# Optimization experiments

Hardware: AMD Instinct MI355X
Metric: run time of the kernel (lower is better)

The kernel has to match this reference:

```python
import jax, jax.numpy as jnp
import numpy as np

B, C, H, W = 64, 64, 64, 64
KD = 64  # kernel_dim == res == dim (required by the torch reshapes)


def _ln(t, g, b, eps=1e-5):
    mu = jnp.mean(t, axis=-1, keepdims=True)
    var = jnp.var(t, axis=-1, keepdims=True)
    return (t - mu) * jax.lax.rsqrt(var + eps) * g + b


def _cos_map(n, kd):
    i = jnp.arange(n, dtype=jnp.float32)[:, None]
    j = jnp.arange(kd, dtype=jnp.float32)[None, :]
    return jnp.cos(i * j * jnp.pi / n) / kd


def setup_inputs() -> dict:
    key = jax.random.key(0)
    ks = jax.random.split(key, 6)
    s = 0.02
    return {
        "x": jax.random.normal(ks[0], (B, C, H, W), jnp.float32),
        "freq_embed": jax.random.normal(ks[1], (H, W, C), jnp.float32),
        "g_k": jnp.ones((C,), jnp.float32), "b_k": jnp.zeros((C,), jnp.float32),
        "Wk": jax.random.normal(ks[2], (C, KD), jnp.float32) * s, "bk": jnp.zeros((KD,), jnp.float32),
        "g_z": jnp.ones((C,), jnp.float32), "b_z": jnp.zeros((C,), jnp.float32),
        "Wz": jax.random.normal(ks[3], (C, C), jnp.float32) * s, "bz": jnp.zeros((C,), jnp.float32),
        "g_o": jnp.ones((KD,), jnp.float32), "b_o": jnp.zeros((KD,), jnp.float32),
        "Wo": jax.random.normal(ks[4], (KD, C), jnp.float32) * s, "bo": jnp.zeros((C,), jnp.float32),
    }


def reference(x, freq_embed, g_k, b_k, Wk, bk, g_z, b_z, Wz, bz, g_o, b_o, Wo, bo):
    # x: (B,C,H,W) -> (B,H,W,C), matching the torch permute branch
    x = jnp.transpose(x, (0, 2, 3, 1))
    Bc, Hc, Wc, Cc = x.shape
    kd = Wk.shape[1]
    xin = x + freq_embed[None]                    # freq_embed broadcast over batch
    k = _ln(xin, g_k, b_k) @ Wk + bk              # (B,H,W,kd)
    z = _ln(freq_embed, g_z, b_z) @ Wz + bz       # to_k(freq_embed): (H,W,C)
    cosn = _cos_map(Hc, kd)                       # (H,kd)
    cosm = _cos_map(Wc, kd)                       # (W,kd)
    i = jnp.arange(Hc, dtype=jnp.float32)[:, None]
    j = jnp.arange(Wc, dtype=jnp.float32)[None, :]
    decay = (jnp.exp(-(i + j) / max(Hc, Wc)) / kd).astype(x.dtype)  # (H,W)
    wexp = decay[:, :, None] ** z                 # (H,W,C), decay > 0
    # separable forward DCT (two kernel-1 conv1d == two contractions)
    t = jnp.einsum('nh,bhwc->bnwc', cosn, k)
    t = jnp.einsum('mw,bnwc->bnmc', cosm, t)
    t = t * wexp[None]                            # exponential-decay spectral gate
    # separable inverse DCT
    t = jnp.einsum('nh,bnmc->bhmc', cosn, t)
    t = jnp.einsum('mw,bhmc->bhwc', cosm, t)
    out = _ln(t, g_o, b_o) * jax.nn.silu(z)[None]
    out = out @ Wo + bo
    return jnp.transpose(out, (0, 3, 1, 2))       # back to BCHW
```

## Files before the change

kernel.cpp:

```cpp
#include <hip/hip_runtime.h>


#define PL_ST 4160
#define TC_ST 4160

typedef __attribute__((ext_vector_type(8))) short short8;
typedef __attribute__((ext_vector_type(4))) float f32x4;
typedef __attribute__((ext_vector_type(4))) unsigned short us4;

__device__ __forceinline__ unsigned short bfhi(float f) {
    return (unsigned short)(__builtin_bit_cast(unsigned int, f) >> 16);
}
__device__ __forceinline__ float hif(float f) {
    return __builtin_bit_cast(float, __builtin_bit_cast(unsigned int, f) & 0xFFFF0000u);
}
__device__ __forceinline__ int swa(int row, int col) {
    return (row << 7) + (((col >> 3) ^ (row & 7)) << 4) + ((col & 7) << 1);
}
__device__ __forceinline__ short8 fragrd(const short* buf, int row, int kc) {
    int a = (row << 7) + ((kc ^ (row & 7)) << 4);
    return *(const short8*)((const char*)buf + a);
}
__device__ __forceinline__ f32x4 mm3(short8 ah, short8 al, short8 bh, short8 bl, f32x4 acc) {
    acc = __builtin_amdgcn_mfma_f32_16x16x32_bf16(ah, bh, acc, 0, 0, 0);
    acc = __builtin_amdgcn_mfma_f32_16x16x32_bf16(ah, bl, acc, 0, 0, 0);
    acc = __builtin_amdgcn_mfma_f32_16x16x32_bf16(al, bh, acc, 0, 0, 0);
    return acc;
}

__device__ __forceinline__ void mm_block(const short* Ah, const short* Al,
                                         const short* Bh, const short* Bl,
                                         int m0, int n0, int l15, int q,
                                         f32x4 (&acc)[2][2]) {
    const f32x4 zero = {0.f, 0.f, 0.f, 0.f};
    acc[0][0] = zero; acc[0][1] = zero; acc[1][0] = zero; acc[1][1] = zero;
    #pragma unroll
    for (int kb = 0; kb < 2; ++kb) {
        int kc = (kb << 2) + q;
        short8 a0h = fragrd(Ah, m0 + l15, kc);
        short8 a0l = fragrd(Al, m0 + l15, kc);
        short8 a1h = fragrd(Ah, m0 + 16 + l15, kc);
        short8 a1l = fragrd(Al, m0 + 16 + l15, kc);
        short8 b0h = fragrd(Bh, n0 + l15, kc);
        short8 b0l = fragrd(Bl, n0 + l15, kc);
        short8 b1h = fragrd(Bh, n0 + 16 + l15, kc);
        short8 b1l = fragrd(Bl, n0 + 16 + l15, kc);
        acc[0][0] = mm3(a0h, a0l, b0h, b0l, acc[0][0]);
        acc[0][1] = mm3(a0h, a0l, b1h, b1l, acc[0][1]);
        acc[1][0] = mm3(a1h, a1l, b0h, b0l, acc[1][0]);
        acc[1][1] = mm3(a1h, a1l, b1h, b1l, acc[1][1]);
    }
}

__device__ __forceinline__ void mm_block_regB(const short* Ah, const short* Al,
                                              const short8 (&bf)[2][2][2],
                                              int m0, int l15, int q,
                                              f32x4 (&acc)[2][2]) {
    const f32x4 zero = {0.f, 0.f, 0.f, 0.f};
    acc[0][0] = zero; acc[0][1] = zero; acc[1][0] = zero; acc[1][1] = zero;
    #pragma unroll
    for (int kb = 0; kb < 2; ++kb) {
        int kc = (kb << 2) + q;
        short8 a0h = fragrd(Ah, m0 + l15, kc);
        short8 a0l = fragrd(Al, m0 + l15, kc);
        short8 a1h = fragrd(Ah, m0 + 16 + l15, kc);
        short8 a1l = fragrd(Al, m0 + 16 + l15, kc);
        #pragma unroll
        for (int u = 0; u < 2; ++u) {
            acc[0][u] = mm3(a0h, a0l, bf[u][kb][0], bf[u][kb][1], acc[0][u]);
            acc[1][u] = mm3(a1h, a1l, bf[u][kb][0], bf[u][kb][1], acc[1][u]);
        }
    }
}

__global__ __launch_bounds__(256) void k_pre1(
    const float* __restrict__ g_k, const float* __restrict__ b_k,
    const float* __restrict__ Wk, const float* __restrict__ bk,
    const float* __restrict__ g_z, const float* __restrict__ b_z,
    const float* __restrict__ Wz, const float* __restrict__ bz,
    const float* __restrict__ Wo,
    unsigned short* __restrict__ WkTh, unsigned short* __restrict__ WkTl,
    float* __restrict__ su_k, float* __restrict__ v_k,
    unsigned short* __restrict__ WzTh, unsigned short* __restrict__ WzTl,
    float* __restrict__ su_z, float* __restrict__ v_z,
    unsigned short* __restrict__ WoTh, unsigned short* __restrict__ WoTl,
    unsigned short* __restrict__ cos_hi, unsigned short* __restrict__ cos_lo) {
    int t = threadIdx.x;
    if (blockIdx.x < 16) {
        int n = blockIdx.x * 4 + (t >> 6);
        int c = t & 63;
        float wk = Wk[c * 64 + n];
        float a = g_k[c] * wk;
        WkTh[n * 64 + c] = bfhi(a);
        WkTl[n * 64 + c] = bfhi(a - hif(a));
        float sa = a, sv = b_k[c] * wk;
        #pragma unroll
        for (int off = 32; off > 0; off >>= 1) {
            sa += __shfl_xor(sa, off, 64);
            sv += __shfl_xor(sv, off, 64);
        }
        if (c == 0) { su_k[n] = sa; v_k[n] = sv + bk[n]; }
        float wz = Wz[c * 64 + n];
        float az = g_z[c] * wz;
        WzTh[n * 64 + c] = bfhi(az);
        WzTl[n * 64 + c] = bfhi(az - hif(az));
        float saz = az, svz = b_z[c] * wz;
        #pragma unroll
        for (int off = 32; off > 0; off >>= 1) {
            saz += __shfl_xor(saz, off, 64);
            svz += __shfl_xor(svz, off, 64);
        }
        if (c == 0) { su_z[n] = saz; v_z[n] = svz + bz[n]; }
        float wo = Wo[c * 64 + n];
        WoTh[n * 64 + c] = bfhi(wo);
        WoTl[n * 64 + c] = bfhi(wo - hif(wo));
    } else {
        int idx = (blockIdx.x - 16) * 256 + t;
        int i = idx >> 6, j = idx & 63;
        float ang = (float)(i * j) * 3.14159265358979323846f * (1.0f / 64.0f);
        float v = cosf(ang) * (1.0f / 64.0f);
        cos_hi[idx] = bfhi(v);
        cos_lo[idx] = bfhi(v - hif(v));
    }
}

__global__ __launch_bounds__(256) void k_pre2(
    const float* __restrict__ freq,
    const unsigned short* __restrict__ WzTh_g, const unsigned short* __restrict__ WzTl_g,
    const float* __restrict__ su_z, const float* __restrict__ v_z,
    float* __restrict__ siluzT, float* __restrict__ wexpT,
    float* __restrict__ freqT) {
    __shared__ __align__(16) short Ah[4096], Al[4096], Bh[4096], Bl[4096];
    __shared__ float muS[64], rsS[64];
    __shared__ float tile[64][65];
    int t = threadIdx.x;
    if (blockIdx.x < 64) {
        int h = blockIdx.x;
        #pragma unroll
        for (int p = 0; p < 2; ++p) {
            int e = t + p * 256;
            int row = e >> 3, ch = e & 7;
            int a = (row << 7) + (((ch ^ (row & 7)) << 4));
            *(uint4*)((char*)Bh + a) = *(const uint4*)&WzTh_g[row * 64 + ch * 8];
            *(uint4*)((char*)Bl + a) = *(const uint4*)&WzTl_g[row * 64 + ch * 8];
        }
        int w = t >> 2, c0 = (t & 3) << 4;
        float4 fr[4];
        float s1 = 0.f, s2 = 0.f;
        #pragma unroll
        for (int i = 0; i < 4; ++i) {
            fr[i] = *(const float4*)&freq[(h * 64 + w) * 64 + c0 + 4 * i];
            s1 += fr[i].x + fr[i].y + fr[i].z + fr[i].w;
            s2 += fr[i].x * fr[i].x + fr[i].y * fr[i].y + fr[i].z * fr[i].z + fr[i].w * fr[i].w;
        }
        s1 += __shfl_xor(s1, 1, 64); s1 += __shfl_xor(s1, 2, 64);
        s2 += __shfl_xor(s2, 1, 64); s2 += __shfl_xor(s2, 2, 64);
        float mu = s1 * (1.0f / 64.0f);
        float var = s2 * (1.0f / 64.0f) - mu * mu;
        float rs = rsqrtf(var + 1e-5f);
        if ((t & 3) == 0) { muS[w] = mu; rsS[w] = rs; }
        const float* fp = (const float*)fr;
        #pragma unroll
        for (int i = 0; i < 4; ++i) {
            us4 hv, lv;
            #pragma unroll
            for (int r = 0; r < 4; ++r) {
                float f = fp[i * 4 + r];
                hv[r] = bfhi(f);
                lv[r] = bfhi(f - hif(f));
            }
            int a = swa(w, c0 + 4 * i);
            *(us4*)((char*)Ah + a) = hv;
            *(us4*)((char*)Al + a) = lv;
        }
        __syncthreads();
        int lane = t & 63, wv = t >> 6;
        int q = lane >> 4, l15 = lane & 15;
        int m0 = (wv & 1) << 5, n0 = (wv >> 1) << 5;
        f32x4 acc[2][2];
        mm_block(Ah, Al, Bh, Bl, m0, n0, l15, q, acc);
        #pragma unroll
        for (int u = 0; u < 2; ++u) {
            int c = n0 + (u << 4) + l15;
            float suc = su_z[c], vc = v_z[c];
            #pragma unroll
            for (int ti = 0; ti < 2; ++ti) {
                int wb = m0 + (ti << 4) + (q << 2);
                float4 mu4 = *(const float4*)&muS[wb];
                float4 rs4 = *(const float4*)&rsS[wb];
                float4 sil, wx;
                #pragma unroll
                for (int r = 0; r < 4; ++r) {
                    float z = ((const float*)&rs4)[r] * (acc[ti][u][r] - ((const float*)&mu4)[r] * suc) + vc;
                    float lnd = -(float)(h + wb + r) * 0.015625f - 4.1588830833596718565f;
                    ((float*)&sil)[r] = z / (1.0f + expf(-z));
                    ((float*)&wx)[r] = expf(z * lnd);
                }
                size_t base = (size_t)c * TC_ST + h * 64 + wb;
                *(float4*)&siluzT[base] = sil;
                *(float4*)&wexpT[base] = wx;
            }
        }
    } else {
        int h = blockIdx.x - 64;
        int w = t >> 2, c0 = (t & 3) << 4;
        #pragma unroll
        for (int i = 0; i < 4; ++i)
            *(float4*)&tile[w][c0 + 4 * i] = *(const float4*)&freq[(h * 64 + w) * 64 + c0 + 4 * i];
        __syncthreads();
        int w0 = (t & 15) << 2;
        #pragma unroll
        for (int p = 0; p < 4; ++p) {
            int c = (t >> 4) + 16 * p;
            float4 fv = make_float4(tile[w0][c], tile[w0 + 1][c], tile[w0 + 2][c], tile[w0 + 3][c]);
            *(float4*)&freqT[(size_t)c * TC_ST + h * 64 + w0] = fv;
        }
    }
}

__global__ __launch_bounds__(256, 3) void k_k(
    const float* __restrict__ x, const float* __restrict__ freqT,
    const unsigned short* __restrict__ WkTh_g, const unsigned short* __restrict__ WkTl_g,
    const float* __restrict__ su_k, const float* __restrict__ v_k,
    float* __restrict__ planes) {
    __shared__ __align__(16) short Ah[2][4096], Al[2][4096];
    __shared__ __align__(16) float red1[4][64], red2[4][64];
    __shared__ float muS[64], rsS[64];
    int b = blockIdx.x >> 4, h0 = (blockIdx.x & 15) << 2;
    int t = threadIdx.x;
    int lane = t & 63, wv = t >> 6;
    int q = lane >> 4, l15 = lane & 15;
    int m0 = (wv & 1) << 5, n0 = (wv >> 1) << 5;
    short8 bf[2][2][2];
    #pragma unroll
    for (int u = 0; u < 2; ++u)
        #pragma unroll
        for (int kb = 0; kb < 2; ++kb) {
            int off = (n0 + (u << 4) + l15) * 64 + ((kb << 2) + q) * 8;
            bf[u][kb][0] = *(const short8*)&WkTh_g[off];
            bf[u][kb][1] = *(const short8*)&WkTl_g[off];
        }
    int g = t >> 4, w0 = (t & 15) << 2, c0 = g << 2;
    const float* xb = x + (size_t)b * 262144;
    float4 xr[2][4], fr[2][4];
    #pragma unroll
    for (int pi = 0; pi < 2; ++pi) {
        int h = h0 + pi;
        #pragma unroll
        for (int i = 0; i < 4; ++i) {
            xr[pi][i] = *(const float4*)&xb[(c0 + i) * 4096 + h * 64 + w0];
            fr[pi][i] = *(const float4*)&freqT[(size_t)(c0 + i) * TC_ST + h * 64 + w0];
        }
    }
    #pragma unroll
    for (int it = 0; it < 4; ++it) {
        int s = it & 1;
        int h = h0 + it;
        float4 vv[4];
        float4 s1 = {0, 0, 0, 0}, s2 = {0, 0, 0, 0};
        #pragma unroll
        for (int i = 0; i < 4; ++i) {
            float4 a = xr[s][i], f = fr[s][i];
            a.x += f.x; a.y += f.y; a.z += f.z; a.w += f.w;
            vv[i] = a;
            s1.x += a.x; s1.y += a.y; s1.z += a.z; s1.w += a.w;
            s2.x += a.x * a.x; s2.y += a.y * a.y; s2.z += a.z * a.z; s2.w += a.w * a.w;
        }
        const float* vp = (const float*)vv;
        #pragma unroll
        for (int j = 0; j < 4; ++j) {
            us4 hv, lv;
            #pragma unroll
            for (int r = 0; r < 4; ++r) {
                float f = vp[r * 4 + j];
                hv[r] = bfhi(f);
                lv[r] = bfhi(f - hif(f));
            }
            int a = swa(w0 + j, c0);
            *(us4*)((char*)Ah[s] + a) = hv;
            *(us4*)((char*)Al[s] + a) = lv;
        }
        #pragma unroll
        for (int r = 0; r < 4; ++r) {
            float a1 = ((const float*)&s1)[r];
            float a2 = ((const float*)&s2)[r];
            a1 += __shfl_xor(a1, 16, 64); a1 += __shfl_xor(a1, 32, 64);
            a2 += __shfl_xor(a2, 16, 64); a2 += __shfl_xor(a2, 32, 64);
            ((float*)&s1)[r] = a1;
            ((float*)&s2)[r] = a2;
        }
        if (lane < 16) {
            *(float4*)&red1[wv][lane << 2] = s1;
            *(float4*)&red2[wv][lane << 2] = s2;
        }
        __syncthreads();
        if (t < 64) {
            float a1 = red1[0][t] + red1[1][t] + red1[2][t] + red1[3][t];
            float a2 = red2[0][t] + red2[1][t] + red2[2][t] + red2[3][t];
            float mu = a1 * (1.0f / 64.0f);
            float var = a2 * (1.0f / 64.0f) - mu * mu;
            muS[t] = mu; rsS[t] = rsqrtf(var + 1e-5f);
        }
        __syncthreads();
        if (it < 2) {
            int hn = h0 + it + 2;
            #pragma unroll
            for (int i = 0; i < 4; ++i) {
                xr[s][i] = *(const float4*)&xb[(c0 + i) * 4096 + hn * 64 + w0];
                fr[s][i] = *(const float4*)&freqT[(size_t)(c0 + i) * TC_ST + hn * 64 + w0];
            }
        }
        f32x4 acc[2][2];
        mm_block_regB(Ah[s], Al[s], bf, m0, l15, q, acc);
        #pragma unroll
        for (int u = 0; u < 2; ++u) {
            int n = n0 + (u << 4) + l15;
            float sun = su_k[n], vn = v_k[n];
            #pragma unroll
            for (int ti = 0; ti < 2; ++ti) {
                int wb = m0 + (ti << 4) + (q << 2);
                float4 mu4 = *(const float4*)&muS[wb];
                float4 rs4 = *(const float4*)&rsS[wb];
                float4 o;
                o.x = rs4.x * (acc[ti][u][0] - mu4.x * sun) + vn;
                o.y = rs4.y * (acc[ti][u][1] - mu4.y * sun) + vn;
                o.z = rs4.z * (acc[ti][u][2] - mu4.z * sun) + vn;
                o.w = rs4.w * (acc[ti][u][3] - mu4.w * sun) + vn;
                *(float4*)&planes[(size_t)(b * 64 + n) * PL_ST + h * 64 + wb] = o;
            }
        }
    }
}

__global__ __launch_bounds__(128, 2) void k_spec(
    float* __restrict__ planes,
    const unsigned short* __restrict__ cos_hi, const unsigned short* __restrict__ cos_lo,
    const float* __restrict__ wexpT) {
    __shared__ __align__(16) short DhS[2][4096], DlS[2][4096];
    int t = threadIdx.x;
    int wv = t >> 6, lane = t & 63;
    int q = lane >> 4, l15 = lane & 15;
    int pid = blockIdx.x * 2 + wv;
    int c = pid & 63;
    float* po = planes + (size_t)pid * PL_ST;
    const float* wx = wexpT + (size_t)c * TC_ST;
    short* dh = DhS[wv];
    short* dl = DlS[wv];

    short8 cf[4][2][2];
    #pragma unroll
    for (int rg = 0; rg < 4; ++rg)
        #pragma unroll
        for (int kb = 0; kb < 2; ++kb) {
            int off = (rg * 16 + l15) * 64 + ((kb << 2) + q) * 8;
            cf[rg][kb][0] = *(const short8*)&cos_hi[off];
            cf[rg][kb][1] = *(const short8*)&cos_lo[off];
        }

    #pragma unroll
    for (int jg = 0; jg < 16; ++jg) {
        float f0 = po[(jg * 4 + 0) * 64 + lane];
        float f1 = po[(jg * 4 + 1) * 64 + lane];
        float f2 = po[(jg * 4 + 2) * 64 + lane];
        float f3 = po[(jg * 4 + 3) * 64 + lane];
        us4 hv, lv;
        hv[0] = bfhi(f0); lv[0] = bfhi(f0 - hif(f0));
        hv[1] = bfhi(f1); lv[1] = bfhi(f1 - hif(f1));
        hv[2] = bfhi(f2); lv[2] = bfhi(f2 - hif(f2));
        hv[3] = bfhi(f3); lv[3] = bfhi(f3 - hif(f3));
        int a = swa(lane, jg << 2);
        *(us4*)((char*)dh + a) = hv;
        *(us4*)((char*)dl + a) = lv;
    }

    short8 af[4][2][2];
    f32x4 acc[2][2];
    const f32x4 zacc = {0.f, 0.f, 0.f, 0.f};

#define LOAD_AF()                                                            \
    _Pragma("unroll")                                                        \
    for (int rg = 0; rg < 4; ++rg) {                                         \
        _Pragma("unroll")                                                    \
        for (int kb = 0; kb < 2; ++kb) {                                     \
            af[rg][kb][0] = fragrd(dh, rg * 16 + l15, (kb << 2) + q);        \
            af[rg][kb][1] = fragrd(dl, rg * 16 + l15, (kb << 2) + q);        \
        }                                                                    \
    }

#define QMM(ASRC, BSRC)                                                      \
    acc[0][0] = zacc; acc[0][1] = zacc; acc[1][0] = zacc; acc[1][1] = zacc;  \
    __builtin_amdgcn_s_setprio(1);                                           \
    _Pragma("unroll")                                                        \
    for (int kb = 0; kb < 2; ++kb)                                           \
        _Pragma("unroll")                                                    \
        for (int ti = 0; ti < 2; ++ti)                                       \
            _Pragma("unroll")                                                \
            for (int u = 0; u < 2; ++u)                                      \
                acc[ti][u] = mm3(ASRC[2 * mq + ti][kb][0], ASRC[2 * mq + ti][kb][1], \
                                 BSRC[2 * nq + u][kb][0], BSRC[2 * nq + u][kb][1],   \
                                 acc[ti][u]);                                \
    __builtin_amdgcn_s_setprio(0);

#define WB_T()                                                               \
    _Pragma("unroll")                                                        \
    for (int ti = 0; ti < 2; ++ti)                                           \
        _Pragma("unroll")                                                    \
        for (int u = 0; u < 2; ++u) {                                        \
            int row = (nq << 5) + (u << 4) + l15;                            \
            int col = (mq << 5) + (ti << 4) + (q << 2);                      \
            int a = swa(row, col);                                           \
            us4 hv, lv;                                                      \
            _Pragma("unroll")                                                \
            for (int r = 0; r < 4; ++r) {                                    \
                float f = acc[ti][u][r];                                     \
                hv[r] = bfhi(f);                                             \
                lv[r] = bfhi(f - hif(f));                                    \
            }                                                                \
            *(us4*)((char*)dh + a) = hv;                                     \
            *(us4*)((char*)dl + a) = lv;                                     \
        }

    LOAD_AF()
    #pragma unroll
    for (int mq = 0; mq < 2; ++mq)
        #pragma unroll
        for (int nq = 0; nq < 2; ++nq) {
            QMM(af, cf)
            WB_T()
        }

    LOAD_AF()
    #pragma unroll
    for (int mq = 0; mq < 2; ++mq)
        #pragma unroll
        for (int nq = 0; nq < 2; ++nq) {
            float wxr[2][2][4];
            #pragma unroll
            for (int ti = 0; ti < 2; ++ti)
                #pragma unroll
                for (int u = 0; u < 2; ++u)
                    #pragma unroll
                    for (int r = 0; r < 4; ++r)
                        wxr[ti][u][r] = wx[((mq << 5) + (ti << 4) + (q << 2) + r) * 64
                                           + (nq << 5) + (u << 4) + l15];
            QMM(af, cf)
            #pragma unroll
            for (int ti = 0; ti < 2; ++ti)
                #pragma unroll
                for (int u = 0; u < 2; ++u)
                    #pragma unroll
                    for (int r = 0; r < 4; ++r)
                        acc[ti][u][r] *= wxr[ti][u][r];
            WB_T()
        }

    LOAD_AF()
    #pragma unroll
    for (int mq = 0; mq < 2; ++mq)
        #pragma unroll
        for (int nq = 0; nq < 2; ++nq) {
            QMM(cf, af)
            #pragma unroll
            for (int ti = 0; ti < 2; ++ti)
                #pragma unroll
                for (int u = 0; u < 2; ++u)
                    #pragma unroll
                    for (int r = 0; r < 4; ++r) {
                        int row = (mq << 5) + (ti << 4) + (q << 2) + r;
                        int col = (nq << 5) + (u << 4) + l15;
                        int a = swa(row, col);
                        float f = acc[ti][u][r];
                        *(unsigned short*)((char*)dh + a) = bfhi(f);
                        *(unsigned short*)((char*)dl + a) = bfhi(f - hif(f));
                    }
        }

    LOAD_AF()
    #pragma unroll
    for (int mq = 0; mq < 2; ++mq)
        #pragma unroll
        for (int nq = 0; nq < 2; ++nq) {
            QMM(af, cf)
            #pragma unroll
            for (int ti = 0; ti < 2; ++ti)
                #pragma unroll
                for (int u = 0; u < 2; ++u)
                    #pragma unroll
                    for (int r = 0; r < 4; ++r) {
                        int h = (mq << 5) + (ti << 4) + (q << 2) + r;
                        int w = (nq << 5) + (u << 4) + l15;
                        po[h * 64 + w] = acc[ti][u][r];
                    }
        }
#undef LOAD_AF
#undef QMM
#undef WB_T
}

__global__ __launch_bounds__(256, 3) void k_out(
    const float* __restrict__ planes, const float* __restrict__ siluzT,
    const float* __restrict__ g_o, const float* __restrict__ b_o,
    const unsigned short* __restrict__ WoTh_g, const unsigned short* __restrict__ WoTl_g,
    const float* __restrict__ bo, float* __restrict__ out) {
    __shared__ __align__(16) short Ah[2][4096], Al[2][4096];
    __shared__ __align__(16) float red1[4][64], red2[4][64];
    __shared__ float muS[64], rsS[64];
    int b = blockIdx.x >> 4, h0 = (blockIdx.x & 15) << 2;
    int t = threadIdx.x;
    int lane = t & 63, wv = t >> 6;
    int q = lane >> 4, l15 = lane & 15;
    int m0 = (wv & 1) << 5, n0 = (wv >> 1) << 5;
    short8 bf[2][2][2];
    #pragma unroll
    for (int u = 0; u < 2; ++u)
        #pragma unroll
        for (int kb = 0; kb < 2; ++kb) {
            int off = (n0 + (u << 4) + l15) * 64 + ((kb << 2) + q) * 8;
            bf[u][kb][0] = *(const short8*)&WoTh_g[off];
            bf[u][kb][1] = *(const short8*)&WoTl_g[off];
        }
    int g = t >> 4, w0 = (t & 15) << 2, c0 = g << 2;
    float4 pr[2][4], sz[2][4];
    #pragma unroll
    for (int pi = 0; pi < 2; ++pi) {
        int h = h0 + pi;
        #pragma unroll
        for (int i = 0; i < 4; ++i) {
            pr[pi][i] = *(const float4*)&planes[(size_t)(b * 64 + c0 + i) * PL_ST + h * 64 + w0];
            sz[pi][i] = *(const float4*)&siluzT[(size_t)(c0 + i) * TC_ST + h * 64 + w0];
        }
    }
    #pragma unroll
    for (int it = 0; it < 4; ++it) {
        int s = it & 1;
        int h = h0 + it;
        float4 s1 = {0, 0, 0, 0}, s2 = {0, 0, 0, 0};
        #pragma unroll
        for (int i = 0; i < 4; ++i) {
            float4 tv = pr[s][i];
            s1.x += tv.x; s1.y += tv.y; s1.z += tv.z; s1.w += tv.w;
            s2.x += tv.x * tv.x; s2.y += tv.y * tv.y;
            s2.z += tv.z * tv.z; s2.w += tv.w * tv.w;
        }
        #pragma unroll
        for (int r = 0; r < 4; ++r) {
            float a1 = ((const float*)&s1)[r];
            float a2 = ((const float*)&s2)[r];
            a1 += __shfl_xor(a1, 16, 64); a1 += __shfl_xor(a1, 32, 64);
            a2 += __shfl_xor(a2, 16, 64); a2 += __shfl_xor(a2, 32, 64);
            ((float*)&s1)[r] = a1;
            ((float*)&s2)[r] = a2;
        }
        if (lane < 16) {
            *(float4*)&red1[wv][lane << 2] = s1;
            *(float4*)&red2[wv][lane << 2] = s2;
        }
        __syncthreads();
        if (t < 64) {
            float a1 = red1[0][t] + red1[1][t] + red1[2][t] + red1[3][t];
            float a2 = red2[0][t] + red2[1][t] + red2[2][t] + red2[3][t];
            float mu = a1 * (1.0f / 64.0f);
            float var = a2 * (1.0f / 64.0f) - mu * mu;
            muS[t] = mu; rsS[t] = rsqrtf(var + 1e-5f);
        }
        __syncthreads();
        {
            float4 mu4 = *(const float4*)&muS[w0];
            float4 rs4 = *(const float4*)&rsS[w0];
            float4 vr[4];
            #pragma unroll
            for (int i = 0; i < 4; ++i) {
                int cc = c0 + i;
                float go = g_o[cc], boc = b_o[cc];
                float4 tv = pr[s][i], sv = sz[s][i];
                vr[i].x = ((tv.x - mu4.x) * rs4.x * go + boc) * sv.x;
                vr[i].y = ((tv.y - mu4.y) * rs4.y * go + boc) * sv.y;
                vr[i].z = ((tv.z - mu4.z) * rs4.z * go + boc) * sv.z;
                vr[i].w = ((tv.w - mu4.w) * rs4.w * go + boc) * sv.w;
            }
            const float* vp = (const float*)vr;
            #pragma unroll
            for (int j = 0; j < 4; ++j) {
                us4 hv, lv;
                #pragma unroll
                for (int r = 0; r < 4; ++r) {
                    float f = vp[r * 4 + j];
                    hv[r] = bfhi(f);
                    lv[r] = bfhi(f - hif(f));
                }
                int a = swa(w0 + j, c0);
                *(us4*)((char*)Ah[s] + a) = hv;
                *(us4*)((char*)Al[s] + a) = lv;
            }
        }
        if (it < 2) {
            int hn = h0 + it + 2;
            #pragma unroll
            for (int i = 0; i < 4; ++i) {
                pr[s][i] = *(const float4*)&planes[(size_t)(b * 64 + c0 + i) * PL_ST + hn * 64 + w0];
                sz[s][i] = *(const float4*)&siluzT[(size_t)(c0 + i) * TC_ST + hn * 64 + w0];
            }
        }
        __syncthreads();
        f32x4 acc[2][2];
        mm_block_regB(Ah[s], Al[s], bf, m0, l15, q, acc);
        #pragma unroll
        for (int u = 0; u < 2; ++u) {
            int o_ = n0 + (u << 4) + l15;
            float bov = bo[o_];
            #pragma unroll
            for (int ti = 0; ti < 2; ++ti) {
                int wb = m0 + (ti << 4) + (q << 2);
                float4 o;
                o.x = acc[ti][u][0] + bov;
                o.y = acc[ti][u][1] + bov;
                o.z = acc[ti][u][2] + bov;
                o.w = acc[ti][u][3] + bov;
                *(float4*)&out[((size_t)(b * 64 + o_) * 64 + h) * 64 + wb] = o;
            }
        }
    }
}

extern "C" void kernel_launch(void* const* d_in, const int* in_sizes, int n_in,
                              void* d_out, int out_size, void* d_ws, size_t ws_size,
                              hipStream_t stream) {
    const float* x    = (const float*)d_in[0];
    const float* freq = (const float*)d_in[1];
    const float* g_k  = (const float*)d_in[2];
    const float* b_k  = (const float*)d_in[3];
    const float* Wk   = (const float*)d_in[4];
    const float* bk   = (const float*)d_in[5];
    const float* g_z  = (const float*)d_in[6];
    const float* b_z  = (const float*)d_in[7];
    const float* Wz   = (const float*)d_in[8];
    const float* bz   = (const float*)d_in[9];
    const float* g_o  = (const float*)d_in[10];
    const float* b_o  = (const float*)d_in[11];
    const float* Wo   = (const float*)d_in[12];
    const float* bo   = (const float*)d_in[13];
    float* out = (float*)d_out;

    float* ws = (float*)d_ws;
    float* planes = ws;
    float* siluzT = planes + (size_t)4096 * PL_ST;
    float* wexpT  = siluzT + (size_t)64 * TC_ST;
    float* freqT  = wexpT + (size_t)64 * TC_ST;
    float* su_k   = freqT + (size_t)64 * TC_ST;
    float* v_k    = su_k + 64;
    float* su_z   = v_k + 64;
    float* v_z    = su_z + 64;
    unsigned short* cos_hi = (unsigned short*)(v_z + 64);
    unsigned short* cos_lo = cos_hi + 4096;
    unsigned short* WkTh = cos_lo + 4096;
    unsigned short* WkTl = WkTh + 4096;
    unsigned short* WzTh = WkTl + 4096;
    unsigned short* WzTl = WzTh + 4096;
    unsigned short* WoTh = WzTl + 4096;
    unsigned short* WoTl = WoTh + 4096;

    k_pre1<<<32, 256, 0, stream>>>(g_k, b_k, Wk, bk, g_z, b_z, Wz, bz, Wo,
                                   WkTh, WkTl, su_k, v_k, WzTh, WzTl, su_z, v_z,
                                   WoTh, WoTl, cos_hi, cos_lo);
    k_pre2<<<128, 256, 0, stream>>>(freq, WzTh, WzTl, su_z, v_z, siluzT, wexpT, freqT);
    k_k<<<1024, 256, 0, stream>>>(x, freqT, WkTh, WkTl, su_k, v_k, planes);
    k_spec<<<2048, 128, 0, stream>>>(planes, cos_hi, cos_lo, wexpT);
    k_out<<<1024, 256, 0, stream>>>(planes, siluzT, g_o, b_o, WoTh, WoTl, bo, out);
}
```

Measured before the change: 233.0 us.

## Split each spectral plane across four waves with shared cosine tiles

```diff
diff --git a/kernel.cpp b/kernel.cpp
--- a/kernel.cpp
+++ b/kernel.cpp
@@ -332,168 +332,181 @@
     }
 }
 
-__global__ __launch_bounds__(128, 2) void k_spec(
+__global__ __launch_bounds__(256, 4) void k_spec(
     float* __restrict__ planes,
     const unsigned short* __restrict__ cos_hi, const unsigned short* __restrict__ cos_lo,
     const float* __restrict__ wexpT) {
-    __shared__ __align__(16) short DhS[2][4096], DlS[2][4096];
+    __shared__ __align__(16) short Ch[4096], Cl[4096];
+    __shared__ __align__(16) short Dh[4096], Dl[4096];
+    int c = blockIdx.x & 63;
+    float* po = planes + (size_t)blockIdx.x * PL_ST;
+    const float* wx = wexpT + (size_t)c * TC_ST;
     int t = threadIdx.x;
-    int wv = t >> 6, lane = t & 63;
+    int lane = t & 63, wv = t >> 6;
     int q = lane >> 4, l15 = lane & 15;
-    int pid = blockIdx.x * 2 + wv;
-    int c = pid & 63;
-    float* po = planes + (size_t)pid * PL_ST;
-    const float* wx = wexpT + (size_t)c * TC_ST;
-    short* dh = DhS[wv];
-    short* dl = DlS[wv];
-
-    short8 cf[4][2][2];
-    #pragma unroll
-    for (int rg = 0; rg < 4; ++rg)
-        #pragma unroll
-        for (int kb = 0; kb < 2; ++kb) {
-            int off = (rg * 16 + l15) * 64 + ((kb << 2) + q) * 8;
-            cf[rg][kb][0] = *(const short8*)&cos_hi[off];
-            cf[rg][kb][1] = *(const short8*)&cos_lo[off];
-        }
-
-    #pragma unroll
-    for (int jg = 0; jg < 16; ++jg) {
-        float f0 = po[(jg * 4 + 0) * 64 + lane];
-        float f1 = po[(jg * 4 + 1) * 64 + lane];
-        float f2 = po[(jg * 4 + 2) * 64 + lane];
-        float f3 = po[(jg * 4 + 3) * 64 + lane];
-        us4 hv, lv;
-        hv[0] = bfhi(f0); lv[0] = bfhi(f0 - hif(f0));
-        hv[1] = bfhi(f1); lv[1] = bfhi(f1 - hif(f1));
-        hv[2] = bfhi(f2); lv[2] = bfhi(f2 - hif(f2));
-        hv[3] = bfhi(f3); lv[3] = bfhi(f3 - hif(f3));
-        int a = swa(lane, jg << 2);
-        *(us4*)((char*)dh + a) = hv;
-        *(us4*)((char*)dl + a) = lv;
-    }
-
-    short8 af[4][2][2];
+    int m0 = (wv & 1) << 5, n0 = (wv >> 1) << 5;
+
+    float wxr[2][2][4];
+    #pragma unroll
+    for (int ti = 0; ti < 2; ++ti)
+        #pragma unroll
+        for (int u = 0; u < 2; ++u)
+            #pragma unroll
+            for (int r = 0; r < 4; ++r)
+                wxr[ti][u][r] = wx[(m0 + (ti << 4) + (q << 2) + r) * 64
+                                   + n0 + (u << 4) + l15];
+
+    {
+        int r = t >> 2, cb = (t & 3) << 4;
+        #pragma unroll
+        for (int p = 0; p < 2; ++p) {
+            int chunk = (cb >> 3) + p;
+            int a = (r << 7) + (((chunk ^ (r & 7)) << 4));
+            *(uint4*)((char*)Ch + a) = *(const uint4*)&cos_hi[r * 64 + cb + p * 8];
+            *(uint4*)((char*)Cl + a) = *(const uint4*)&cos_lo[r * 64 + cb + p * 8];
+        }
+    }
+    {
+        int w = t & 63, h0 = (t >> 6) << 4;
+        float v[16];
+        #pragma unroll
+        for (int j = 0; j < 16; ++j) v[j] = po[(h0 + j) * 64 + w];
+        #pragma unroll
+        for (int gg = 0; gg < 4; ++gg) {
+            int col = h0 + (gg << 2);
+            int a = swa(w, col);
+            us4 hv, lv;
+            #pragma unroll
+            for (int r = 0; r < 4; ++r) {
+                float f = v[(gg << 2) + r];
+                hv[r] = bfhi(f);
+                lv[r] = bfhi(f - hif(f));
+            }
+            *(us4*)((char*)Dh + a) = hv;
+            *(us4*)((char*)Dl + a) = lv;
+        }
+    }
+    __syncthreads();
+
+    short8 af[2][2][2];
     f32x4 acc[2][2];
     const f32x4 zacc = {0.f, 0.f, 0.f, 0.f};
 
-#define LOAD_AF()                                                            \
-    _Pragma("unroll")                                                        \
-    for (int rg = 0; rg < 4; ++rg) {                                         \
-        _Pragma("unroll")                                                    \
-        for (int kb = 0; kb < 2; ++kb) {                                     \
-            af[rg][kb][0] = fragrd(dh, rg * 16 + l15, (kb << 2) + q);        \
-            af[rg][kb][1] = fragrd(dl, rg * 16 + l15, (kb << 2) + q);        \
-        }                                                                    \
-    }
-
-#define QMM(ASRC, BSRC)                                                      \
-    acc[0][0] = zacc; acc[0][1] = zacc; acc[1][0] = zacc; acc[1][1] = zacc;  \
-    __builtin_amdgcn_s_setprio(1);                                           \
-    _Pragma("unroll")                                                        \
-    for (int kb = 0; kb < 2; ++kb)                                           \
-        _Pragma("unroll")                                                    \
-        for (int ti = 0; ti < 2; ++ti)                                       \
-            _Pragma("unroll")                                                \
-            for (int u = 0; u < 2; ++u)                                      \
-                acc[ti][u] = mm3(ASRC[2 * mq + ti][kb][0], ASRC[2 * mq + ti][kb][1], \
-                                 BSRC[2 * nq + u][kb][0], BSRC[2 * nq + u][kb][1],   \
-                                 acc[ti][u]);                                \
+#define LOAD_D(base)                                                          \
+    _Pragma("unroll")                                                         \
+    for (int tt = 0; tt < 2; ++tt)                                            \
+        _Pragma("unroll")                                                     \
+        for (int kb = 0; kb < 2; ++kb) {                                      \
+            af[tt][kb][0] = fragrd(Dh, (base) + (tt << 4) + l15, (kb << 2) + q); \
+            af[tt][kb][1] = fragrd(Dl, (base) + (tt << 4) + l15, (kb << 2) + q); \
+        }
+
+#define QMM_AC()                                                              \
+    acc[0][0] = zacc; acc[0][1] = zacc; acc[1][0] = zacc; acc[1][1] = zacc;   \
+    __builtin_amdgcn_s_setprio(1);                                            \
+    _Pragma("unroll")                                                         \
+    for (int kb = 0; kb < 2; ++kb) {                                          \
+        int kc = (kb << 2) + q;                                               \
+        short8 b0h = fragrd(Ch, n0 + l15, kc);                                \
+        short8 b0l = fragrd(Cl, n0 + l15, kc);                                \
+        short8 b1h = fragrd(Ch, n0 + 16 + l15, kc);                           \
+        short8 b1l = fragrd(Cl, n0 + 16 + l15, kc);                           \
+        acc[0][0] = mm3(af[0][kb][0], af[0][kb][1], b0h, b0l, acc[0][0]);     \
+        acc[0][1] = mm3(af[0][kb][0], af[0][kb][1], b1h, b1l, acc[0][1]);     \
+        acc[1][0] = mm3(af[1][kb][0], af[1][kb][1], b0h, b0l, acc[1][0]);     \
+        acc[1][1] = mm3(af[1][kb][0], af[1][kb][1], b1h, b1l, acc[1][1]);     \
+    }                                                                         \
     __builtin_amdgcn_s_setprio(0);
 
-#define WB_T()                                                               \
-    _Pragma("unroll")                                                        \
-    for (int ti = 0; ti < 2; ++ti)                                           \
-        _Pragma("unroll")                                                    \
-        for (int u = 0; u < 2; ++u) {                                        \
-            int row = (nq << 5) + (u << 4) + l15;                            \
-            int col = (mq << 5) + (ti << 4) + (q << 2);                      \
-            int a = swa(row, col);                                           \
-            us4 hv, lv;                                                      \
-            _Pragma("unroll")                                                \
-            for (int r = 0; r < 4; ++r) {                                    \
-                float f = acc[ti][u][r];                                     \
-                hv[r] = bfhi(f);                                             \
-                lv[r] = bfhi(f - hif(f));                                    \
-            }                                                                \
-            *(us4*)((char*)dh + a) = hv;                                     \
-            *(us4*)((char*)dl + a) = lv;                                     \
-        }
-
-    LOAD_AF()
-    #pragma unroll
-    for (int mq = 0; mq < 2; ++mq)
-        #pragma unroll
-        for (int nq = 0; nq < 2; ++nq) {
-            QMM(af, cf)
-            WB_T()
-        }
-
-    LOAD_AF()
-    #pragma unroll
-    for (int mq = 0; mq < 2; ++mq)
-        #pragma unroll
-        for (int nq = 0; nq < 2; ++nq) {
-            float wxr[2][2][4];
-            #pragma unroll
-            for (int ti = 0; ti < 2; ++ti)
-                #pragma unroll
-                for (int u = 0; u < 2; ++u)
-                    #pragma unroll
-                    for (int r = 0; r < 4; ++r)
-                        wxr[ti][u][r] = wx[((mq << 5) + (ti << 4) + (q << 2) + r) * 64
-                                           + (nq << 5) + (u << 4) + l15];
-            QMM(af, cf)
-            #pragma unroll
-            for (int ti = 0; ti < 2; ++ti)
-                #pragma unroll
-                for (int u = 0; u < 2; ++u)
-                    #pragma unroll
-                    for (int r = 0; r < 4; ++r)
-                        acc[ti][u][r] *= wxr[ti][u][r];
-            WB_T()
-        }
-
-    LOAD_AF()
-    #pragma unroll
-    for (int mq = 0; mq < 2; ++mq)
-        #pragma unroll
-        for (int nq = 0; nq < 2; ++nq) {
-            QMM(cf, af)
-            #pragma unroll
-            for (int ti = 0; ti < 2; ++ti)
-                #pragma unroll
-                for (int u = 0; u < 2; ++u)
-                    #pragma unroll
-                    for (int r = 0; r < 4; ++r) {
-                        int row = (mq << 5) + (ti << 4) + (q << 2) + r;
-                        int col = (nq << 5) + (u << 4) + l15;
-                        int a = swa(row, col);
-                        float f = acc[ti][u][r];
-                        *(unsigned short*)((char*)dh + a) = bfhi(f);
-                        *(unsigned short*)((char*)dl + a) = bfhi(f - hif(f));
-                    }
-        }
-
-    LOAD_AF()
-    #pragma unroll
-    for (int mq = 0; mq < 2; ++mq)
-        #pragma unroll
-        for (int nq = 0; nq < 2; ++nq) {
-            QMM(af, cf)
-            #pragma unroll
-            for (int ti = 0; ti < 2; ++ti)
-                #pragma unroll
-                for (int u = 0; u < 2; ++u)
-                    #pragma unroll
-                    for (int r = 0; r < 4; ++r) {
-                        int h = (mq << 5) + (ti << 4) + (q << 2) + r;
-                        int w = (nq << 5) + (u << 4) + l15;
-                        po[h * 64 + w] = acc[ti][u][r];
-                    }
-        }
-#undef LOAD_AF
-#undef QMM
+#define QMM_CA()                                                              \
+    acc[0][0] = zacc; acc[0][1] = zacc; acc[1][0] = zacc; acc[1][1] = zacc;   \
+    __builtin_amdgcn_s_setprio(1);                                            \
+    _Pragma("unroll")                                                         \
+    for (int kb = 0; kb < 2; ++kb) {                                          \
+        int kc = (kb << 2) + q;                                               \
+        short8 a0h = fragrd(Ch, m0 + l15, kc);                                \
+        short8 a0l = fragrd(Cl, m0 + l15, kc);                                \
+        short8 a1h = fragrd(Ch, m0 + 16 + l15, kc);                           \
+        short8 a1l = fragrd(Cl, m0 + 16 + l15, kc);                           \
+        acc[0][0] = mm3(a0h, a0l, af[0][kb][0], af[0][kb][1], acc[0][0]);     \
+        acc[0][1] = mm3(a0h, a0l, af[1][kb][0], af[1][kb][1], acc[0][1]);     \
+        acc[1][0] = mm3(a1h, a1l, af[0][kb][0], af[0][kb][1], acc[1][0]);     \
+        acc[1][1] = mm3(a1h, a1l, af[1][kb][0], af[1][kb][1], acc[1][1]);     \
+    }                                                                         \
+    __builtin_amdgcn_s_setprio(0);
+
+#define WB_T()                                                                \
+    _Pragma("unroll")                                                         \
+    for (int ti = 0; ti < 2; ++ti)                                            \
+        _Pragma("unroll")                                                     \
+        for (int u = 0; u < 2; ++u) {                                         \
+            int row = n0 + (u << 4) + l15;                                    \
+            int col = m0 + (ti << 4) + (q << 2);                              \
+            int a = swa(row, col);                                            \
+            us4 hv, lv;                                                       \
+            _Pragma("unroll")                                                 \
+            for (int r = 0; r < 4; ++r) {                                     \
+                float f = acc[ti][u][r];                                      \
+                hv[r] = bfhi(f);                                              \
+                lv[r] = bfhi(f - hif(f));                                     \
+            }                                                                 \
+            *(us4*)((char*)Dh + a) = hv;                                      \
+            *(us4*)((char*)Dl + a) = lv;                                      \
+        }
+
+    LOAD_D(m0)
+    __syncthreads();
+    QMM_AC()
+    WB_T()
+    __syncthreads();
+
+    LOAD_D(m0)
+    __syncthreads();
+    QMM_AC()
+    #pragma unroll
+    for (int ti = 0; ti < 2; ++ti)
+        #pragma unroll
+        for (int u = 0; u < 2; ++u)
+            #pragma unroll
+            for (int r = 0; r < 4; ++r)
+                acc[ti][u][r] *= wxr[ti][u][r];
+    WB_T()
+    __syncthreads();
+
+    LOAD_D(n0)
+    __syncthreads();
+    QMM_CA()
+    #pragma unroll
+    for (int ti = 0; ti < 2; ++ti)
+        #pragma unroll
+        for (int u = 0; u < 2; ++u)
+            #pragma unroll
+            for (int r = 0; r < 4; ++r) {
+                int row = m0 + (ti << 4) + (q << 2) + r;
+                int col = n0 + (u << 4) + l15;
+                int a = swa(row, col);
+                float f = acc[ti][u][r];
+                *(unsigned short*)((char*)Dh + a) = bfhi(f);
+                *(unsigned short*)((char*)Dl + a) = bfhi(f - hif(f));
+            }
+    __syncthreads();
+
+    LOAD_D(m0)
+    __syncthreads();
+    QMM_AC()
+    #pragma unroll
+    for (int ti = 0; ti < 2; ++ti)
+        #pragma unroll
+        for (int u = 0; u < 2; ++u)
+            #pragma unroll
+            for (int r = 0; r < 4; ++r) {
+                int h = m0 + (ti << 4) + (q << 2) + r;
+                int w = n0 + (u << 4) + l15;
+                po[h * 64 + w] = acc[ti][u][r];
+            }
+#undef LOAD_D
+#undef QMM_AC
+#undef QMM_CA
 #undef WB_T
 }
 
@@ -664,6 +677,6 @@
                                    WoTh, WoTl, cos_hi, cos_lo);
     k_pre2<<<128, 256, 0, stream>>>(freq, WzTh, WzTl, su_z, v_z, siluzT, wexpT, freqT);
     k_k<<<1024, 256, 0, stream>>>(x, freqT, WkTh, WkTl, su_k, v_k, planes);
-    k_spec<<<2048, 128, 0, stream>>>(planes, cos_hi, cos_lo, wexpT);
+    k_spec<<<4096, 256, 0, stream>>>(planes, cos_hi, cos_lo, wexpT);
     k_out<<<1024, 256, 0, stream>>>(planes, siluzT, g_o, b_o, WoTh, WoTl, bo, out);
 }
```

New measurement: 228.8 us. About the same (-1.8%).
